# Kernel optimization log

Hardware: AMD Instinct MI355X
Metric: run time of the kernel (lower is better)

## Reference

```python
import jax, jax.numpy as jnp
import numpy as np

N_V, N_E, N_F = 6000, 12000, 8000
D_IN, D_OUT = 32, 32


def _glorot(key, shape):
    lim = float(np.sqrt(6.0 / (shape[0] + shape[1])))
    return jax.random.uniform(key, shape, jnp.float32, -lim, lim)


def setup_inputs() -> dict:
    key = jax.random.key(0)
    ks = jax.random.split(key, 13)
    return {
        "xv": jax.random.normal(ks[0], (N_V, D_IN), jnp.float32),
        "xe": jax.random.normal(ks[1], (N_E, D_IN), jnp.float32),
        "xf": jax.random.normal(ks[2], (N_F, D_IN), jnp.float32),
        "Gv2v": jax.random.normal(ks[3], (N_V, N_V), jnp.float32) / np.sqrt(N_V),
        "Gv2e": jax.random.normal(ks[4], (N_E, N_V), jnp.float32) / np.sqrt(N_V),
        "Ge2e": jax.random.normal(ks[5], (N_E, N_E), jnp.float32) / np.sqrt(N_E),
        "Ge2f": jax.random.normal(ks[6], (N_F, N_E), jnp.float32) / np.sqrt(N_E),
        "Gf2f": jax.random.normal(ks[7], (N_F, N_F), jnp.float32) / np.sqrt(N_F),
        "Wv2v": _glorot(ks[8], (D_IN, D_OUT)),
        "Wv2e": _glorot(ks[9], (D_IN, D_OUT)),
        "We2e": _glorot(ks[10], (D_IN, D_OUT)),
        "We2f": _glorot(ks[11], (D_IN, D_OUT)),
        "Wf2f": _glorot(ks[12], (D_IN, D_OUT)),
    }


def reference(xv, xe, xf, Gv2v, Gv2e, Ge2e, Ge2f, Gf2f,
              Wv2v, Wv2e, We2e, We2f, Wf2f):
    # Eval mode: dropout is identity. activation=None -> no nonlinearity.
    # LTN(x, G) = G @ (x @ W); MergeOper = sum of two LTNs.
    zv = Gv2v @ (xv @ Wv2v)                               # [n_v, d_out]
    ze = Gv2e @ (xv @ Wv2e) + Ge2e @ (xe @ We2e)          # [n_e, d_out]
    zf = Ge2f @ (xe @ We2f) + Gf2f @ (xf @ Wf2f)          # [n_f, d_out]
    return zv, ze, zf
```

## Files before the change

### kernel.cpp

```cpp
#include <hip/hip_runtime.h>

typedef float  f32x4 __attribute__((ext_vector_type(4)));
typedef short  s16x8 __attribute__((ext_vector_type(8)));

#define PK   256
#define PSTR 260

typedef const __attribute__((address_space(1))) float* gas1f;
typedef __attribute__((address_space(3))) float*       las3f;

__device__ __forceinline__ short f2bf(float f) {
  unsigned u = __builtin_bit_cast(unsigned, f);
  u += 0x7FFFu + ((u >> 16) & 1u);
  return (short)(u >> 16);
}

__global__ __launch_bounds__(256) void build_yt(
    const float* __restrict__ xv, const float* __restrict__ xe,
    const float* __restrict__ xf,
    const float* __restrict__ Wv2v, const float* __restrict__ Wv2e,
    const float* __restrict__ We2e, const float* __restrict__ We2f,
    const float* __restrict__ Wf2f, short* __restrict__ Yt)
{
  int bid = blockIdx.x;
  const float* x; const float* W; int K, Kpad; size_t yoff;
  if (bid < 24)       { x=xv; W=Wv2v; K=6000;  Kpad=6144;  yoff=0;       }
  else if (bid < 48)  { x=xv; W=Wv2e; K=6000;  Kpad=6144;  yoff=196608;  bid-=24; }
  else if (bid < 95)  { x=xe; W=We2e; K=12000; Kpad=12032; yoff=393216;  bid-=48; }
  else if (bid < 142) { x=xe; W=We2f; K=12000; Kpad=12032; yoff=778240;  bid-=95; }
  else                { x=xf; W=Wf2f; K=8000;  Kpad=8192;  yoff=1163264; bid-=142; }

  __shared__ float Wl[32][32];
  int tid = threadIdx.x;
  #pragma unroll
  for (int i = 0; i < 4; ++i) {
    int e = tid + i * 256;
    Wl[e >> 5][e & 31] = W[e];
  }
  __syncthreads();

  int row = bid * 256 + tid;
  if (row >= Kpad) return;

  float acc[32];
  #pragma unroll
  for (int c = 0; c < 32; ++c) acc[c] = 0.f;

  if (row < K) {
    const float* xp = x + (size_t)row * 32;
    float xr[32];
    #pragma unroll
    for (int i = 0; i < 8; ++i) {
      f32x4 v = *(const f32x4*)(xp + i * 4);
      xr[i*4+0] = v.x; xr[i*4+1] = v.y; xr[i*4+2] = v.z; xr[i*4+3] = v.w;
    }
    #pragma unroll
    for (int d = 0; d < 32; ++d) {
      float xd = xr[d];
      #pragma unroll
      for (int c = 0; c < 32; ++c) acc[c] += xd * Wl[d][c];
    }
  }
  #pragma unroll
  for (int c = 0; c < 32; ++c)
    Yt[yoff + (size_t)c * Kpad + row] = f2bf(acc[c]);
}

__device__ __forceinline__ void stage_panel(
    const float* __restrict__ G, int K, int row0, int pn, int lane, int w,
    float (*panel)[16][PSTR], int bb)
{
  if ((pn + 1) * PK <= K) {
    const float* base = G + (size_t)row0 * K + (size_t)pn * PK;
    #pragma unroll
    for (int j = 0; j < 4; ++j) {
      int rr = 4 * w + j;
      __builtin_amdgcn_global_load_lds((gas1f)(base + (size_t)rr * K + lane * 4),
                                       (las3f)&panel[bb][rr][0], 16, 0, 2 );
    }
  } else {
    #pragma unroll
    for (int j = 0; j < 4; ++j) {
      int rr = 4 * w + j;
      int k = pn * PK + lane * 4;
      f32x4 v = {0.f, 0.f, 0.f, 0.f};
      if (k < K) v = *(const f32x4*)(G + (size_t)(row0 + rr) * K + k);
      *(f32x4*)&panel[bb][rr][lane * 4] = v;
    }
  }
}

__device__ __forceinline__ void seg_run(
    const float* __restrict__ G, const short* __restrict__ Yt,
    int K, int Kpad, int row0, int lane, int w,
    float (*panel)[16][PSTR], f32x4& acc0, f32x4& acc1)
{
  int np = (K + PK - 1) / PK;
  int r = lane & 15, g = lane >> 4;

  stage_panel(G, K, row0, 0, lane, w, panel, 0);
  stage_panel(G, K, row0, 1, lane, w, panel, 1);

  for (int p = 0; p < np; ++p) {
    if (p + 1 < np && (p + 2) * PK <= K)
      asm volatile("s_waitcnt vmcnt(4)" ::: "memory");
    else
      asm volatile("s_waitcnt vmcnt(0)" ::: "memory");
    __builtin_amdgcn_s_barrier();

    int b = p & 1;
    #pragma unroll
    for (int si = 0; si < 2; ++si) {
      int s  = 2 * w + si;
      int kk = s * 32 + g * 8;
      f32x4 a0 = *(const f32x4*)&panel[b][r][kk];
      f32x4 a1 = *(const f32x4*)&panel[b][r][kk + 4];
      s16x8 a;
      a[0] = f2bf(a0.x); a[1] = f2bf(a0.y); a[2] = f2bf(a0.z); a[3] = f2bf(a0.w);
      a[4] = f2bf(a1.x); a[5] = f2bf(a1.y); a[6] = f2bf(a1.z); a[7] = f2bf(a1.w);
      int kg = p * PK + kk;
      s16x8 vb0 = *(const s16x8*)(Yt + (size_t)r * Kpad + kg);
      s16x8 vb1 = *(const s16x8*)(Yt + (size_t)(r + 16) * Kpad + kg);
      acc0 = __builtin_amdgcn_mfma_f32_16x16x32_bf16(a, vb0, acc0, 0, 0, 0);
      acc1 = __builtin_amdgcn_mfma_f32_16x16x32_bf16(a, vb1, acc1, 0, 0, 0);
    }

    asm volatile("s_waitcnt lgkmcnt(0)" ::: "memory");
    __builtin_amdgcn_sched_barrier(0);
    __builtin_amdgcn_s_barrier();
    if (p + 2 < np) stage_panel(G, K, row0, p + 2, lane, w, panel, b);
  }
  __syncthreads();
}

__global__ __launch_bounds__(256) void gemm_skinny(
    const float* __restrict__ Gv2v, const float* __restrict__ Gv2e,
    const float* __restrict__ Ge2e, const float* __restrict__ Ge2f,
    const float* __restrict__ Gf2f, const short* __restrict__ Yt,
    float* __restrict__ out)
{
  __shared__ float panel[2][16][PSTR];

  int bid  = blockIdx.x;
  int lane = threadIdx.x & 63, w = threadIdx.x >> 6;

  const float *G0, *G1; const short *Y0, *Y1;
  int K0, Kp0, K1, Kp1, tile; size_t ob;
  if (bid < 500) {
    tile = bid;
    G0 = Ge2f; Y0 = Yt + 778240;  K0 = 12000; Kp0 = 12032;
    G1 = Gf2f; Y1 = Yt + 1163264; K1 = 8000;  Kp1 = 8192;
    ob = (size_t)18000 * 32;
  } else if (bid < 1250) {
    tile = bid - 500;
    G0 = Gv2e; Y0 = Yt + 196608;  K0 = 6000;  Kp0 = 6144;
    G1 = Ge2e; Y1 = Yt + 393216;  K1 = 12000; Kp1 = 12032;
    ob = (size_t)6000 * 32;
  } else {
    tile = bid - 1250;
    G0 = Gv2v; Y0 = Yt;           K0 = 6000;  Kp0 = 6144;
    G1 = nullptr; Y1 = nullptr;   K1 = 0; Kp1 = 0;
    ob = 0;
  }
  int row0 = tile * 16;

  f32x4 acc0 = {0.f,0.f,0.f,0.f}, acc1 = {0.f,0.f,0.f,0.f};
  seg_run(G0, Y0, K0, Kp0, row0, lane, w, panel, acc0, acc1);
  if (G1) seg_run(G1, Y1, K1, Kp1, row0, lane, w, panel, acc0, acc1);

  float (*red)[512] = (float (*)[512])panel;
  int r = lane & 15, g = lane >> 4;
  #pragma unroll
  for (int q = 0; q < 4; ++q) {
    int rw = g * 4 + q;
    red[w][rw * 32 + r]      = acc0[q];
    red[w][rw * 32 + 16 + r] = acc1[q];
  }
  __syncthreads();
  #pragma unroll
  for (int i = 0; i < 2; ++i) {
    int e = (int)threadIdx.x + i * 256;
    float s = red[0][e] + red[1][e] + red[2][e] + red[3][e];
    out[ob + (size_t)row0 * 32 + e] = s;
  }
}

extern "C" void kernel_launch(void* const* d_in, const int* in_sizes, int n_in,
                              void* d_out, int out_size, void* d_ws, size_t ws_size,
                              hipStream_t stream) {
  const float* xv   = (const float*)d_in[0];
  const float* xe   = (const float*)d_in[1];
  const float* xf   = (const float*)d_in[2];
  const float* Gv2v = (const float*)d_in[3];
  const float* Gv2e = (const float*)d_in[4];
  const float* Ge2e = (const float*)d_in[5];
  const float* Ge2f = (const float*)d_in[6];
  const float* Gf2f = (const float*)d_in[7];
  const float* Wv2v = (const float*)d_in[8];
  const float* Wv2e = (const float*)d_in[9];
  const float* We2e = (const float*)d_in[10];
  const float* We2f = (const float*)d_in[11];
  const float* Wf2f = (const float*)d_in[12];
  short* Yt  = (short*)d_ws;
  float* out = (float*)d_out;

  hipLaunchKernelGGL(build_yt, dim3(174), dim3(256), 0, stream,
                     xv, xe, xf, Wv2v, Wv2e, We2e, We2f, Wf2f, Yt);
  hipLaunchKernelGGL(gemm_skinny, dim3(1625), dim3(256), 0, stream,
                     Gv2v, Gv2e, Ge2e, Ge2f, Gf2f, Yt, out);
}
```

Baseline: 356.3 us.

## Merge segment loops, prefetch Yt fragments, and swizzle LDS panel instead of padding

The two per-tile GEMM segments now run as one continuous double-buffered panel loop, so the pipeline no longer drains between segments. The bf16 Yt operand fragments for the next panel are loaded into registers one iteration ahead, overlapping their latency with the current MFMAs. The LDS panel padding is replaced by an XOR swizzle on the DMA source address, which shrinks shared memory, and launch bounds now request 5 blocks per CU to raise occupancy. Since the kernel streams G from HBM and is likely already bandwidth-bound, the gain may be limited, and the added index logic adds some scalar overhead.

```diff
diff --git a/kernel.cpp b/kernel.cpp
--- a/kernel.cpp
+++ b/kernel.cpp
@@ -3,8 +3,7 @@
 typedef float  f32x4 __attribute__((ext_vector_type(4)));
 typedef short  s16x8 __attribute__((ext_vector_type(8)));
 
-#define PK   256
-#define PSTR 260
+#define PK 256
 
 typedef const __attribute__((address_space(1))) float* gas1f;
 typedef __attribute__((address_space(3))) float*       las3f;
@@ -66,110 +65,143 @@
     Yt[yoff + (size_t)c * Kpad + row] = f2bf(acc[c]);
 }
 
-__device__ __forceinline__ void stage_panel(
-    const float* __restrict__ G, int K, int row0, int pn, int lane, int w,
-    float (*panel)[16][PSTR], int bb)
+struct SegD { const float* G; const short* Y; int K, Kp, np; };
+
+__device__ __forceinline__ void resolve(const SegD& s0, const SegD& s1, int idx,
+                                        const SegD*& s, int& pn) {
+  if (idx < s0.np) { s = &s0; pn = idx; }
+  else             { s = &s1; pn = idx - s0.np; }
+}
+
+__device__ __forceinline__ int dma4(const SegD& s0, const SegD& s1, int idx, int npT) {
+  if (idx >= npT) return 0;
+  const SegD* s; int pn; resolve(s0, s1, idx, s, pn);
+  return ((pn + 1) * PK <= s->K) ? 4 : 0;
+}
+
+__device__ __forceinline__ void stage_idx(
+    const SegD& s0, const SegD& s1, int idx, int npT, int row0, int lane, int w,
+    float (*panel)[16][PK])
 {
-  if ((pn + 1) * PK <= K) {
-    const float* base = G + (size_t)row0 * K + (size_t)pn * PK;
+  if (idx >= npT) return;
+  const SegD* s; int pn; resolve(s0, s1, idx, s, pn);
+  int bb = idx & 1;
+  if ((pn + 1) * PK <= s->K) {
     #pragma unroll
     for (int j = 0; j < 4; ++j) {
       int rr = 4 * w + j;
-      __builtin_amdgcn_global_load_lds((gas1f)(base + (size_t)rr * K + lane * 4),
+      const float* src = s->G + (size_t)(row0 + rr) * s->K + pn * PK
+                       + ((lane ^ (rr & 7)) << 2);
+      __builtin_amdgcn_global_load_lds((gas1f)src,
                                        (las3f)&panel[bb][rr][0], 16, 0, 2 );
     }
   } else {
     #pragma unroll
     for (int j = 0; j < 4; ++j) {
       int rr = 4 * w + j;
-      int k = pn * PK + lane * 4;
+      int k = pn * PK + ((lane ^ (rr & 7)) << 2);
       f32x4 v = {0.f, 0.f, 0.f, 0.f};
-      if (k < K) v = *(const f32x4*)(G + (size_t)(row0 + rr) * K + k);
-      *(f32x4*)&panel[bb][rr][lane * 4] = v;
-    }
-  }
-}
-
-__device__ __forceinline__ void seg_run(
-    const float* __restrict__ G, const short* __restrict__ Yt,
-    int K, int Kpad, int row0, int lane, int w,
-    float (*panel)[16][PSTR], f32x4& acc0, f32x4& acc1)
-{
-  int np = (K + PK - 1) / PK;
-  int r = lane & 15, g = lane >> 4;
-
-  stage_panel(G, K, row0, 0, lane, w, panel, 0);
-  stage_panel(G, K, row0, 1, lane, w, panel, 1);
-
-  for (int p = 0; p < np; ++p) {
-    if (p + 1 < np && (p + 2) * PK <= K)
-      asm volatile("s_waitcnt vmcnt(4)" ::: "memory");
-    else
-      asm volatile("s_waitcnt vmcnt(0)" ::: "memory");
-    __builtin_amdgcn_s_barrier();
-
-    int b = p & 1;
-    #pragma unroll
-    for (int si = 0; si < 2; ++si) {
-      int s  = 2 * w + si;
-      int kk = s * 32 + g * 8;
-      f32x4 a0 = *(const f32x4*)&panel[b][r][kk];
-      f32x4 a1 = *(const f32x4*)&panel[b][r][kk + 4];
-      s16x8 a;
-      a[0] = f2bf(a0.x); a[1] = f2bf(a0.y); a[2] = f2bf(a0.z); a[3] = f2bf(a0.w);
-      a[4] = f2bf(a1.x); a[5] = f2bf(a1.y); a[6] = f2bf(a1.z); a[7] = f2bf(a1.w);
-      int kg = p * PK + kk;
-      s16x8 vb0 = *(const s16x8*)(Yt + (size_t)r * Kpad + kg);
-      s16x8 vb1 = *(const s16x8*)(Yt + (size_t)(r + 16) * Kpad + kg);
-      acc0 = __builtin_amdgcn_mfma_f32_16x16x32_bf16(a, vb0, acc0, 0, 0, 0);
-      acc1 = __builtin_amdgcn_mfma_f32_16x16x32_bf16(a, vb1, acc1, 0, 0, 0);
-    }
-
-    asm volatile("s_waitcnt lgkmcnt(0)" ::: "memory");
-    __builtin_amdgcn_sched_barrier(0);
-    __builtin_amdgcn_s_barrier();
-    if (p + 2 < np) stage_panel(G, K, row0, p + 2, lane, w, panel, b);
-  }
-  __syncthreads();
-}
-
-__global__ __launch_bounds__(256) void gemm_skinny(
+      if (k < s->K) v = *(const f32x4*)(s->G + (size_t)(row0 + rr) * s->K + k);
+      *(f32x4*)&panel[bb][rr][lane << 2] = v;
+    }
+  }
+}
+
+__global__ __launch_bounds__(256, 5) void gemm_skinny(
     const float* __restrict__ Gv2v, const float* __restrict__ Gv2e,
     const float* __restrict__ Ge2e, const float* __restrict__ Ge2f,
     const float* __restrict__ Gf2f, const short* __restrict__ Yt,
     float* __restrict__ out)
 {
-  __shared__ float panel[2][16][PSTR];
+  __shared__ float panel[2][16][PK];
 
   int bid  = blockIdx.x;
   int lane = threadIdx.x & 63, w = threadIdx.x >> 6;
-
-  const float *G0, *G1; const short *Y0, *Y1;
-  int K0, Kp0, K1, Kp1, tile; size_t ob;
+  int r = lane & 15, g = lane >> 4;
+
+  SegD s0, s1; size_t ob; int tile;
   if (bid < 500) {
     tile = bid;
-    G0 = Ge2f; Y0 = Yt + 778240;  K0 = 12000; Kp0 = 12032;
-    G1 = Gf2f; Y1 = Yt + 1163264; K1 = 8000;  Kp1 = 8192;
+    s0 = { Ge2f, Yt + 778240,  12000, 12032, 47 };
+    s1 = { Gf2f, Yt + 1163264, 8000,  8192,  32 };
     ob = (size_t)18000 * 32;
   } else if (bid < 1250) {
     tile = bid - 500;
-    G0 = Gv2e; Y0 = Yt + 196608;  K0 = 6000;  Kp0 = 6144;
-    G1 = Ge2e; Y1 = Yt + 393216;  K1 = 12000; Kp1 = 12032;
+    s0 = { Gv2e, Yt + 196608,  6000,  6144,  24 };
+    s1 = { Ge2e, Yt + 393216,  12000, 12032, 47 };
     ob = (size_t)6000 * 32;
   } else {
     tile = bid - 1250;
-    G0 = Gv2v; Y0 = Yt;           K0 = 6000;  Kp0 = 6144;
-    G1 = nullptr; Y1 = nullptr;   K1 = 0; Kp1 = 0;
+    s0 = { Gv2v, Yt,           6000,  6144,  24 };
+    s1 = { nullptr, nullptr,   0,     0,     0  };
     ob = 0;
   }
+  int npT  = s0.np + s1.np;
   int row0 = tile * 16;
 
+  stage_idx(s0, s1, 0, npT, row0, lane, w, panel);
+  s16x8 B0a, B0b, B1a, B1b;
+  {
+    const SegD* sc; int pn; resolve(s0, s1, 0, sc, pn);
+    int kg0 = pn * PK + (2 * w + 0) * 32 + g * 8;
+    int kg1 = pn * PK + (2 * w + 1) * 32 + g * 8;
+    B0a = *(const s16x8*)(sc->Y + (size_t)r        * sc->Kp + kg0);
+    B0b = *(const s16x8*)(sc->Y + (size_t)(r + 16) * sc->Kp + kg0);
+    B1a = *(const s16x8*)(sc->Y + (size_t)r        * sc->Kp + kg1);
+    B1b = *(const s16x8*)(sc->Y + (size_t)(r + 16) * sc->Kp + kg1);
+  }
+  stage_idx(s0, s1, 1, npT, row0, lane, w, panel);
+
   f32x4 acc0 = {0.f,0.f,0.f,0.f}, acc1 = {0.f,0.f,0.f,0.f};
-  seg_run(G0, Y0, K0, Kp0, row0, lane, w, panel, acc0, acc1);
-  if (G1) seg_run(G1, Y1, K1, Kp1, row0, lane, w, panel, acc0, acc1);
+
+  for (int p = 0; p < npT; ++p) {
+    if (dma4(s0, s1, p + 1, npT))
+      asm volatile("s_waitcnt vmcnt(4)" ::: "memory");
+    else
+      asm volatile("s_waitcnt vmcnt(0)" ::: "memory");
+    __builtin_amdgcn_s_barrier();
+
+    s16x8 N0a, N0b, N1a, N1b;
+    bool have_next = (p + 1 < npT);
+    if (have_next) {
+      const SegD* sn; int pn1; resolve(s0, s1, p + 1, sn, pn1);
+      int kg0 = pn1 * PK + (2 * w + 0) * 32 + g * 8;
+      int kg1 = pn1 * PK + (2 * w + 1) * 32 + g * 8;
+      N0a = *(const s16x8*)(sn->Y + (size_t)r        * sn->Kp + kg0);
+      N0b = *(const s16x8*)(sn->Y + (size_t)(r + 16) * sn->Kp + kg0);
+      N1a = *(const s16x8*)(sn->Y + (size_t)r        * sn->Kp + kg1);
+      N1b = *(const s16x8*)(sn->Y + (size_t)(r + 16) * sn->Kp + kg1);
+    }
+
+    int b  = p & 1;
+    int sw = r & 7;
+    const float* rowp = &panel[b][r][0];
+    #pragma unroll
+    for (int si = 0; si < 2; ++si) {
+      int c0 = (2 * w + si) * 8 + g * 2;
+      f32x4 a0 = *(const f32x4*)(rowp + (((c0    ) ^ sw) << 2));
+      f32x4 a1 = *(const f32x4*)(rowp + (((c0 + 1) ^ sw) << 2));
+      s16x8 a;
+      a[0] = f2bf(a0.x); a[1] = f2bf(a0.y); a[2] = f2bf(a0.z); a[3] = f2bf(a0.w);
+      a[4] = f2bf(a1.x); a[5] = f2bf(a1.y); a[6] = f2bf(a1.z); a[7] = f2bf(a1.w);
+      if (si == 0) {
+        acc0 = __builtin_amdgcn_mfma_f32_16x16x32_bf16(a, B0a, acc0, 0, 0, 0);
+        acc1 = __builtin_amdgcn_mfma_f32_16x16x32_bf16(a, B0b, acc1, 0, 0, 0);
+      } else {
+        acc0 = __builtin_amdgcn_mfma_f32_16x16x32_bf16(a, B1a, acc0, 0, 0, 0);
+        acc1 = __builtin_amdgcn_mfma_f32_16x16x32_bf16(a, B1b, acc1, 0, 0, 0);
+      }
+    }
+
+    asm volatile("s_waitcnt lgkmcnt(0)" ::: "memory");
+    __builtin_amdgcn_sched_barrier(0);
+    __builtin_amdgcn_s_barrier();
+    stage_idx(s0, s1, p + 2, npT, row0, lane, w, panel);
+
+    if (have_next) { B0a = N0a; B0b = N0b; B1a = N1a; B1b = N1b; }
+  }
 
   float (*red)[512] = (float (*)[512])panel;
-  int r = lane & 15, g = lane >> 4;
   #pragma unroll
   for (int q = 0; q < 4; ++q) {
     int rw = g * 4 + q;
```

Measured after the change: 376.3 us. 5.6% more time.

## Double K panel depth and prefetch Y operand into registers one panel ahead

Applied to the files above, without the earlier changes.

Raises the staged G panel depth from 256 to 512 columns, so each panel now takes two global-to-LDS loads per row, and re-pads the Yt workspace to match. The Yt (B operand) fragments for the next panel are loaded into registers while the current panel is computed, which moves their latency off the MFMA critical path. Launch bounds now request 2 blocks per CU, and the doubled LDS panel buffer costs occupancy and adds register pressure from the Bc and Bn arrays.

```diff
diff --git a/kernel.cpp b/kernel.cpp
--- a/kernel.cpp
+++ b/kernel.cpp
@@ -3,8 +3,8 @@
 typedef float  f32x4 __attribute__((ext_vector_type(4)));
 typedef short  s16x8 __attribute__((ext_vector_type(8)));
 
-#define PK   256
-#define PSTR 260
+#define PK   512
+#define PSTR 516
 
 typedef const __attribute__((address_space(1))) float* gas1f;
 typedef __attribute__((address_space(3))) float*       las3f;
@@ -26,9 +26,9 @@
   const float* x; const float* W; int K, Kpad; size_t yoff;
   if (bid < 24)       { x=xv; W=Wv2v; K=6000;  Kpad=6144;  yoff=0;       }
   else if (bid < 48)  { x=xv; W=Wv2e; K=6000;  Kpad=6144;  yoff=196608;  bid-=24; }
-  else if (bid < 95)  { x=xe; W=We2e; K=12000; Kpad=12032; yoff=393216;  bid-=48; }
-  else if (bid < 142) { x=xe; W=We2f; K=12000; Kpad=12032; yoff=778240;  bid-=95; }
-  else                { x=xf; W=Wf2f; K=8000;  Kpad=8192;  yoff=1163264; bid-=142; }
+  else if (bid < 96)  { x=xe; W=We2e; K=12000; Kpad=12288; yoff=393216;  bid-=48; }
+  else if (bid < 144) { x=xe; W=We2f; K=12000; Kpad=12288; yoff=786432;  bid-=96; }
+  else                { x=xf; W=Wf2f; K=8000;  Kpad=8192;  yoff=1179648; bid-=144; }
 
   __shared__ float Wl[32][32];
   int tid = threadIdx.x;
@@ -71,69 +71,92 @@
     float (*panel)[16][PSTR], int bb)
 {
   if ((pn + 1) * PK <= K) {
-    const float* base = G + (size_t)row0 * K + (size_t)pn * PK;
     #pragma unroll
     for (int j = 0; j < 4; ++j) {
       int rr = 4 * w + j;
-      __builtin_amdgcn_global_load_lds((gas1f)(base + (size_t)rr * K + lane * 4),
-                                       (las3f)&panel[bb][rr][0], 16, 0, 2 );
+      const float* base = G + (size_t)(row0 + rr) * K + pn * PK;
+      __builtin_amdgcn_global_load_lds((gas1f)(base + lane * 4),
+                                       (las3f)&panel[bb][rr][0],   16, 0, 2);
+      __builtin_amdgcn_global_load_lds((gas1f)(base + 256 + lane * 4),
+                                       (las3f)&panel[bb][rr][256], 16, 0, 2);
     }
   } else {
     #pragma unroll
     for (int j = 0; j < 4; ++j) {
       int rr = 4 * w + j;
-      int k = pn * PK + lane * 4;
-      f32x4 v = {0.f, 0.f, 0.f, 0.f};
-      if (k < K) v = *(const f32x4*)(G + (size_t)(row0 + rr) * K + k);
-      *(f32x4*)&panel[bb][rr][lane * 4] = v;
-    }
+      #pragma unroll
+      for (int h = 0; h < 2; ++h) {
+        int k = pn * PK + h * 256 + lane * 4;
+        f32x4 v = {0.f, 0.f, 0.f, 0.f};
+        if (k < K) v = *(const f32x4*)(G + (size_t)(row0 + rr) * K + k);
+        *(f32x4*)&panel[bb][rr][h * 256 + lane * 4] = v;
+      }
+    }
+  }
+}
+
+__device__ __forceinline__ void loadB(const short* __restrict__ Y, int Kp,
+                                      int r, int g, int w, int p, s16x8 B[4][2])
+{
+  #pragma unroll
+  for (int si = 0; si < 4; ++si) {
+    int kg = p * PK + (4 * w + si) * 32 + g * 8;
+    B[si][0] = *(const s16x8*)(Y + (size_t)r        * Kp + kg);
+    B[si][1] = *(const s16x8*)(Y + (size_t)(r + 16) * Kp + kg);
   }
 }
 
 __device__ __forceinline__ void seg_run(
     const float* __restrict__ G, const short* __restrict__ Yt,
-    int K, int Kpad, int row0, int lane, int w,
+    int K, int Kp, int np, int row0, int lane, int w,
     float (*panel)[16][PSTR], f32x4& acc0, f32x4& acc1)
 {
-  int np = (K + PK - 1) / PK;
   int r = lane & 15, g = lane >> 4;
+  s16x8 Bc[4][2], Bn[4][2];
 
   stage_panel(G, K, row0, 0, lane, w, panel, 0);
-  stage_panel(G, K, row0, 1, lane, w, panel, 1);
+  loadB(Yt, Kp, r, g, w, 0, Bc);
+  if (np > 1) stage_panel(G, K, row0, 1, lane, w, panel, 1);
 
   for (int p = 0; p < np; ++p) {
     if (p + 1 < np && (p + 2) * PK <= K)
-      asm volatile("s_waitcnt vmcnt(4)" ::: "memory");
+      asm volatile("s_waitcnt vmcnt(8)" ::: "memory");
     else
       asm volatile("s_waitcnt vmcnt(0)" ::: "memory");
     __builtin_amdgcn_s_barrier();
 
     int b = p & 1;
-    #pragma unroll
-    for (int si = 0; si < 2; ++si) {
-      int s  = 2 * w + si;
-      int kk = s * 32 + g * 8;
-      f32x4 a0 = *(const f32x4*)&panel[b][r][kk];
-      f32x4 a1 = *(const f32x4*)&panel[b][r][kk + 4];
+    const float* rowp = &panel[b][r][0];
+    #pragma unroll
+    for (int si = 0; si < 4; ++si) {
+      int kk = (4 * w + si) * 32 + g * 8;
+      f32x4 a0 = *(const f32x4*)(rowp + kk);
+      f32x4 a1 = *(const f32x4*)(rowp + kk + 4);
       s16x8 a;
       a[0] = f2bf(a0.x); a[1] = f2bf(a0.y); a[2] = f2bf(a0.z); a[3] = f2bf(a0.w);
       a[4] = f2bf(a1.x); a[5] = f2bf(a1.y); a[6] = f2bf(a1.z); a[7] = f2bf(a1.w);
-      int kg = p * PK + kk;
-      s16x8 vb0 = *(const s16x8*)(Yt + (size_t)r * Kpad + kg);
-      s16x8 vb1 = *(const s16x8*)(Yt + (size_t)(r + 16) * Kpad + kg);
-      acc0 = __builtin_amdgcn_mfma_f32_16x16x32_bf16(a, vb0, acc0, 0, 0, 0);
-      acc1 = __builtin_amdgcn_mfma_f32_16x16x32_bf16(a, vb1, acc1, 0, 0, 0);
-    }
+      acc0 = __builtin_amdgcn_mfma_f32_16x16x32_bf16(a, Bc[si][0], acc0, 0, 0, 0);
+      acc1 = __builtin_amdgcn_mfma_f32_16x16x32_bf16(a, Bc[si][1], acc1, 0, 0, 0);
+    }
+
+    if (p + 1 < np) loadB(Yt, Kp, r, g, w, p + 1, Bn);
 
     asm volatile("s_waitcnt lgkmcnt(0)" ::: "memory");
     __builtin_amdgcn_sched_barrier(0);
     __builtin_amdgcn_s_barrier();
     if (p + 2 < np) stage_panel(G, K, row0, p + 2, lane, w, panel, b);
+
+    if (p + 1 < np) {
+      #pragma unroll
+      for (int si = 0; si < 4; ++si) {
+        Bc[si][0] = Bn[si][0]; Bc[si][1] = Bn[si][1];
+      }
+    }
   }
   __syncthreads();
 }
 
-__global__ __launch_bounds__(256) void gemm_skinny(
+__global__ __launch_bounds__(256, 2) void gemm_skinny(
     const float* __restrict__ Gv2v, const float* __restrict__ Gv2e,
     const float* __restrict__ Ge2e, const float* __restrict__ Ge2f,
     const float* __restrict__ Gf2f, const short* __restrict__ Yt,
@@ -145,28 +168,28 @@
   int lane = threadIdx.x & 63, w = threadIdx.x >> 6;
 
   const float *G0, *G1; const short *Y0, *Y1;
-  int K0, Kp0, K1, Kp1, tile; size_t ob;
+  int K0, Kp0, n0, K1, Kp1, n1, tile; size_t ob;
   if (bid < 500) {
     tile = bid;
-    G0 = Ge2f; Y0 = Yt + 778240;  K0 = 12000; Kp0 = 12032;
-    G1 = Gf2f; Y1 = Yt + 1163264; K1 = 8000;  Kp1 = 8192;
+    G0 = Ge2f; Y0 = Yt + 786432;  K0 = 12000; Kp0 = 12288; n0 = 24;
+    G1 = Gf2f; Y1 = Yt + 1179648; K1 = 8000;  Kp1 = 8192;  n1 = 16;
     ob = (size_t)18000 * 32;
   } else if (bid < 1250) {
     tile = bid - 500;
-    G0 = Gv2e; Y0 = Yt + 196608;  K0 = 6000;  Kp0 = 6144;
-    G1 = Ge2e; Y1 = Yt + 393216;  K1 = 12000; Kp1 = 12032;
+    G0 = Gv2e; Y0 = Yt + 196608;  K0 = 6000;  Kp0 = 6144;  n0 = 12;
+    G1 = Ge2e; Y1 = Yt + 393216;  K1 = 12000; Kp1 = 12288; n1 = 24;
     ob = (size_t)6000 * 32;
   } else {
     tile = bid - 1250;
-    G0 = Gv2v; Y0 = Yt;           K0 = 6000;  Kp0 = 6144;
-    G1 = nullptr; Y1 = nullptr;   K1 = 0; Kp1 = 0;
+    G0 = Gv2v; Y0 = Yt;           K0 = 6000;  Kp0 = 6144;  n0 = 12;
+    G1 = nullptr; Y1 = nullptr;   K1 = 0; Kp1 = 0; n1 = 0;
     ob = 0;
   }
   int row0 = tile * 16;
 
   f32x4 acc0 = {0.f,0.f,0.f,0.f}, acc1 = {0.f,0.f,0.f,0.f};
-  seg_run(G0, Y0, K0, Kp0, row0, lane, w, panel, acc0, acc1);
-  if (G1) seg_run(G1, Y1, K1, Kp1, row0, lane, w, panel, acc0, acc1);
+  seg_run(G0, Y0, K0, Kp0, n0, row0, lane, w, panel, acc0, acc1);
+  if (G1) seg_run(G1, Y1, K1, Kp1, n1, row0, lane, w, panel, acc0, acc1);
 
   float (*red)[512] = (float (*)[512])panel;
   int r = lane & 15, g = lane >> 4;
@@ -204,7 +227,7 @@
   short* Yt  = (short*)d_ws;
   float* out = (float*)d_out;
 
-  hipLaunchKernelGGL(build_yt, dim3(174), dim3(256), 0, stream,
+  hipLaunchKernelGGL(build_yt, dim3(176), dim3(256), 0, stream,
                      xv, xe, xf, Wv2v, Wv2e, We2e, We2f, Wf2f, Yt);
   hipLaunchKernelGGL(gemm_skinny, dim3(1625), dim3(256), 0, stream,
                      Gv2v, Gv2e, Ge2e, Ge2f, Gf2f, Yt, out);
```

New measurement: 362.8 us. Within noise of the previous version (+1.8%).

## Split-K the skinny GEMM into balanced chunks with a partial-sum reduce kernel

Applied to the files above, without the earlier changes.

Splits each output tile's K range into roughly equal chunks of about 16-24 panels, so 4625 blocks each do similar work instead of 1625 blocks of very uneven length. Partial sums go to workspace and a new reduce kernel adds them into the output. It also prefetches the bf16 B operand one panel ahead in registers and changes the cache-policy bits on the global-to-LDS loads. The cost is an extra launch, extra partial-sum traffic, and more per-block prologue and epilogue overhead.

```diff
diff --git a/kernel.cpp b/kernel.cpp
--- a/kernel.cpp
+++ b/kernel.cpp
@@ -76,7 +76,7 @@
     for (int j = 0; j < 4; ++j) {
       int rr = 4 * w + j;
       __builtin_amdgcn_global_load_lds((gas1f)(base + (size_t)rr * K + lane * 4),
-                                       (las3f)&panel[bb][rr][0], 16, 0, 2 );
+                                       (las3f)&panel[bb][rr][0], 16, 0, 0);
     }
   } else {
     #pragma unroll
@@ -90,45 +90,64 @@
   }
 }
 
+__device__ __forceinline__ void loadB(const short* __restrict__ Y, int Kp,
+                                      int r, int g, int w, int p, s16x8 B[2][2])
+{
+  #pragma unroll
+  for (int si = 0; si < 2; ++si) {
+    int kg = p * PK + (2 * w + si) * 32 + g * 8;
+    B[si][0] = *(const s16x8*)(Y + (size_t)r        * Kp + kg);
+    B[si][1] = *(const s16x8*)(Y + (size_t)(r + 16) * Kp + kg);
+  }
+}
+
 __device__ __forceinline__ void seg_run(
     const float* __restrict__ G, const short* __restrict__ Yt,
-    int K, int Kpad, int row0, int lane, int w,
+    int K, int Kp, int row0, int p_lo, int p_hi, int lane, int w,
     float (*panel)[16][PSTR], f32x4& acc0, f32x4& acc1)
 {
-  int np = (K + PK - 1) / PK;
   int r = lane & 15, g = lane >> 4;
-
-  stage_panel(G, K, row0, 0, lane, w, panel, 0);
-  stage_panel(G, K, row0, 1, lane, w, panel, 1);
-
-  for (int p = 0; p < np; ++p) {
-    if (p + 1 < np && (p + 2) * PK <= K)
+  s16x8 Bc[2][2], Bn[2][2];
+
+  stage_panel(G, K, row0, p_lo, lane, w, panel, p_lo & 1);
+  loadB(Yt, Kp, r, g, w, p_lo, Bc);
+  if (p_lo + 1 < p_hi) stage_panel(G, K, row0, p_lo + 1, lane, w, panel, (p_lo + 1) & 1);
+
+  for (int p = p_lo; p < p_hi; ++p) {
+    if (p + 1 < p_hi && (p + 2) * PK <= K)
       asm volatile("s_waitcnt vmcnt(4)" ::: "memory");
     else
       asm volatile("s_waitcnt vmcnt(0)" ::: "memory");
     __builtin_amdgcn_s_barrier();
 
     int b = p & 1;
+    const float* rowp = &panel[b][r][0];
     #pragma unroll
     for (int si = 0; si < 2; ++si) {
-      int s  = 2 * w + si;
-      int kk = s * 32 + g * 8;
-      f32x4 a0 = *(const f32x4*)&panel[b][r][kk];
-      f32x4 a1 = *(const f32x4*)&panel[b][r][kk + 4];
+      int kk = (2 * w + si) * 32 + g * 8;
+      f32x4 a0 = *(const f32x4*)(rowp + kk);
+      f32x4 a1 = *(const f32x4*)(rowp + kk + 4);
       s16x8 a;
       a[0] = f2bf(a0.x); a[1] = f2bf(a0.y); a[2] = f2bf(a0.z); a[3] = f2bf(a0.w);
       a[4] = f2bf(a1.x); a[5] = f2bf(a1.y); a[6] = f2bf(a1.z); a[7] = f2bf(a1.w);
-      int kg = p * PK + kk;
-      s16x8 vb0 = *(const s16x8*)(Yt + (size_t)r * Kpad + kg);
-      s16x8 vb1 = *(const s16x8*)(Yt + (size_t)(r + 16) * Kpad + kg);
-      acc0 = __builtin_amdgcn_mfma_f32_16x16x32_bf16(a, vb0, acc0, 0, 0, 0);
-      acc1 = __builtin_amdgcn_mfma_f32_16x16x32_bf16(a, vb1, acc1, 0, 0, 0);
-    }
+      acc0 = __builtin_amdgcn_mfma_f32_16x16x32_bf16(a, Bc[si][0], acc0, 0, 0, 0);
+      acc1 = __builtin_amdgcn_mfma_f32_16x16x32_bf16(a, Bc[si][1], acc1, 0, 0, 0);
+    }
+
+    bool have_next = (p + 1 < p_hi);
+    if (have_next) loadB(Yt, Kp, r, g, w, p + 1, Bn);
 
     asm volatile("s_waitcnt lgkmcnt(0)" ::: "memory");
     __builtin_amdgcn_sched_barrier(0);
     __builtin_amdgcn_s_barrier();
-    if (p + 2 < np) stage_panel(G, K, row0, p + 2, lane, w, panel, b);
+    if (p + 2 < p_hi) stage_panel(G, K, row0, p + 2, lane, w, panel, b);
+
+    if (have_next) {
+      #pragma unroll
+      for (int si = 0; si < 2; ++si) {
+        Bc[si][0] = Bn[si][0]; Bc[si][1] = Bn[si][1];
+      }
+    }
   }
   __syncthreads();
 }
@@ -137,36 +156,40 @@
     const float* __restrict__ Gv2v, const float* __restrict__ Gv2e,
     const float* __restrict__ Ge2e, const float* __restrict__ Ge2f,
     const float* __restrict__ Gf2f, const short* __restrict__ Yt,
-    float* __restrict__ out)
+    float* __restrict__ part, float* __restrict__ out)
 {
   __shared__ float panel[2][16][PSTR];
 
   int bid  = blockIdx.x;
   int lane = threadIdx.x & 63, w = threadIdx.x >> 6;
 
-  const float *G0, *G1; const short *Y0, *Y1;
-  int K0, Kp0, K1, Kp1, tile; size_t ob;
-  if (bid < 500) {
-    tile = bid;
-    G0 = Ge2f; Y0 = Yt + 778240;  K0 = 12000; Kp0 = 12032;
-    G1 = Gf2f; Y1 = Yt + 1163264; K1 = 8000;  Kp1 = 8192;
-    ob = (size_t)18000 * 32;
-  } else if (bid < 1250) {
-    tile = bid - 500;
-    G0 = Gv2e; Y0 = Yt + 196608;  K0 = 6000;  Kp0 = 6144;
-    G1 = Ge2e; Y1 = Yt + 393216;  K1 = 12000; Kp1 = 12032;
-    ob = (size_t)6000 * 32;
+  const float* G; const short* Y; int K, Kp, p_lo, p_hi, tile;
+  float* dst;
+  if (bid < 2000) {
+    tile = bid >> 2; int c = bid & 3;
+    if (c < 2) { G = Ge2f; Y = Yt + 778240;  K = 12000; Kp = 12032;
+                 p_lo = c ? 24 : 0;        p_hi = c ? 47 : 24; }
+    else       { G = Gf2f; Y = Yt + 1163264; K = 8000;  Kp = 8192;
+                 p_lo = (c == 3) ? 16 : 0; p_hi = (c == 3) ? 32 : 16; }
+    dst = (c == 0) ? out + 576000 + (size_t)tile * 512
+                   : part + (size_t)(tile * 3 + (c - 1)) * 512;
+  } else if (bid < 4250) {
+    int t2 = bid - 2000; tile = t2 / 3; int c = t2 - tile * 3;
+    if (c == 0) { G = Gv2e; Y = Yt + 196608; K = 6000;  Kp = 6144;
+                  p_lo = 0;  p_hi = 24; }
+    else        { G = Ge2e; Y = Yt + 393216; K = 12000; Kp = 12032;
+                  p_lo = (c == 2) ? 24 : 0; p_hi = (c == 2) ? 47 : 24; }
+    dst = (c == 0) ? out + 192000 + (size_t)tile * 512
+                   : part + (size_t)(1500 + tile * 2 + (c - 1)) * 512;
   } else {
-    tile = bid - 1250;
-    G0 = Gv2v; Y0 = Yt;           K0 = 6000;  Kp0 = 6144;
-    G1 = nullptr; Y1 = nullptr;   K1 = 0; Kp1 = 0;
-    ob = 0;
+    tile = bid - 4250;
+    G = Gv2v; Y = Yt; K = 6000; Kp = 6144; p_lo = 0; p_hi = 24;
+    dst = out + (size_t)tile * 512;
   }
   int row0 = tile * 16;
 
   f32x4 acc0 = {0.f,0.f,0.f,0.f}, acc1 = {0.f,0.f,0.f,0.f};
-  seg_run(G0, Y0, K0, Kp0, row0, lane, w, panel, acc0, acc1);
-  if (G1) seg_run(G1, Y1, K1, Kp1, row0, lane, w, panel, acc0, acc1);
+  seg_run(G, Y, K, Kp, row0, p_lo, p_hi, lane, w, panel, acc0, acc1);
 
   float (*red)[512] = (float (*)[512])panel;
   int r = lane & 15, g = lane >> 4;
@@ -180,8 +203,23 @@
   #pragma unroll
   for (int i = 0; i < 2; ++i) {
     int e = (int)threadIdx.x + i * 256;
-    float s = red[0][e] + red[1][e] + red[2][e] + red[3][e];
-    out[ob + (size_t)row0 * 32 + e] = s;
+    dst[e] = red[0][e] + red[1][e] + red[2][e] + red[3][e];
+  }
+}
+
+__global__ __launch_bounds__(256) void reduce_partials(
+    float* __restrict__ out, const float* __restrict__ part)
+{
+  int e = blockIdx.x * 256 + threadIdx.x;
+  if (e < 256000) {
+    int tile = e >> 9, wi = e & 511;
+    const float* p = part + (size_t)tile * 3 * 512;
+    out[576000 + e] += p[wi] + p[512 + wi] + p[1024 + wi];
+  } else if (e < 640000) {
+    int e2 = e - 256000;
+    int t = e2 >> 9, wi = e2 & 511;
+    const float* p = part + (size_t)(1500 + t * 2) * 512;
+    out[192000 + e2] += p[wi] + p[512 + wi];
   }
 }
 
@@ -201,11 +239,14 @@
   const float* We2e = (const float*)d_in[10];
   const float* We2f = (const float*)d_in[11];
   const float* Wf2f = (const float*)d_in[12];
-  short* Yt  = (short*)d_ws;
-  float* out = (float*)d_out;
+  short* Yt   = (short*)d_ws;
+  float* part = (float*)((char*)d_ws + 2850816);
+  float* out  = (float*)d_out;
 
   hipLaunchKernelGGL(build_yt, dim3(174), dim3(256), 0, stream,
                      xv, xe, xf, Wv2v, Wv2e, We2e, We2f, Wf2f, Yt);
-  hipLaunchKernelGGL(gemm_skinny, dim3(1625), dim3(256), 0, stream,
-                     Gv2v, Gv2e, Ge2e, Ge2f, Gf2f, Yt, out);
-}
+  hipLaunchKernelGGL(gemm_skinny, dim3(4625), dim3(256), 0, stream,
+                     Gv2v, Gv2e, Ge2e, Ge2f, Gf2f, Yt, part, out);
+  hipLaunchKernelGGL(reduce_partials, dim3(2500), dim3(256), 0, stream,
+                     out, part);
+}
```

Result: slower. 384.9 us (+8.0%).
